# Optimization experiments

Hardware: AMD Instinct MI355X
Metric: run time of the kernel (lower is better)

The kernel has to match this reference:

```python
import jax, jax.numpy as jnp
import numpy as np

NUM_HEADS = 8
HEAD_DIM = 32  # in_channels // num_heads = 256 // 8


def setup_inputs() -> dict:
    key = jax.random.key(0)
    k1, k2, k3, k4 = jax.random.split(key, 4)
    B, C, H, W = 16, 256, 64, 64
    N = (H // 2) * (W // 2)  # 1024
    return {
        "x": jax.random.normal(k1, (B, C, H, W), dtype=jnp.float32),
        "w_qkv": jax.random.normal(k2, (3 * C, C), dtype=jnp.float32) * (1.0 / np.sqrt(C)),
        "b_qkv": jax.random.normal(k3, (3 * C,), dtype=jnp.float32) * 0.02,
        "pos_encoding": jax.random.normal(k4, (1, N, HEAD_DIM), dtype=jnp.float32) * 0.02,
    }


def reference(x, w_qkv, b_qkv, pos_encoding):
    B, C, H, W = x.shape
    Hp, Wp = H // 2, W // 2
    N = Hp * Wp
    # 1x1 conv: [B,C,H,W] -> [B,3C,H,W]
    y = jnp.einsum('bchw,oc->bohw', x, w_qkv) + b_qkv[None, :, None, None]
    # 2x2 max pool, stride 2
    y = y.reshape(B, 3 * C, Hp, 2, Wp, 2).max(axis=(3, 5))  # [B,3C,Hp,Wp]
    # split into q,k,v heads: channel order is (3, heads, head_dim)
    qkv = y.reshape(B, 3, NUM_HEADS, HEAD_DIM, N)
    qkv = qkv.transpose(1, 0, 2, 4, 3)  # [3,B,h,N,d]
    q, k, v = qkv[0], qkv[1], qkv[2]
    q = q + pos_encoding[:, None, :, :]  # broadcast over heads -> [B,h,N,d]
    scale = HEAD_DIM ** (-0.5)
    attn = jnp.einsum('bhnd,bhmd->bhnm', q, k) * scale
    attn = jax.nn.softmax(attn, axis=-1)
    out = jnp.einsum('bhnm,bhmd->bhnd', attn, v)  # [B,h,N,d]
    # transpose(2,3) then reshape -> [B, C, Hp, Wp]
    out = out.transpose(0, 1, 3, 2).reshape(B, C, Hp, Wp)
    return out
```

## Files before the change

### kernel.cpp

```cpp
#include <hip/hip_runtime.h>
#include <hip/hip_bf16.h>

typedef __bf16 bf16;
typedef bf16 bf16x8 __attribute__((ext_vector_type(8)));
typedef float f32x4 __attribute__((ext_vector_type(4)));
typedef float f32x16 __attribute__((ext_vector_type(16)));
typedef unsigned int u32;
typedef u32 u32x2 __attribute__((ext_vector_type(2)));
typedef u32 u32x4 __attribute__((ext_vector_type(4)));
typedef int i32x2 __attribute__((ext_vector_type(2)));


__device__ __forceinline__ u32 packbf2(float lo, float hi) {
    unsigned short a = __builtin_bit_cast(unsigned short, (bf16)lo);
    unsigned short b = __builtin_bit_cast(unsigned short, (bf16)hi);
    return (u32)a | ((u32)b << 16);
}

#if __has_builtin(__builtin_amdgcn_exp2f)
#define EXP2(x) __builtin_amdgcn_exp2f(x)
#else
#define EXP2(x) __expf((x)*0.69314718055994531f)
#endif

__device__ __forceinline__ i32x2 pl32swap(u32 a, u32 b) {
#if __has_builtin(__builtin_amdgcn_permlane32_swap)
    return __builtin_amdgcn_permlane32_swap((int)a, (int)b, false, false);
#else
    int lid = __builtin_amdgcn_mbcnt_hi(~0u, __builtin_amdgcn_mbcnt_lo(~0u, 0));
    u32 ax = (u32)__shfl_xor((int)a, 32);
    u32 bx = (u32)__shfl_xor((int)b, 32);
    i32x2 r;
    r.x = (int)(lid < 32 ? a : bx);
    r.y = (int)(lid < 32 ? ax : b);
    return r;
#endif
}

__device__ __forceinline__ f32x16 zero16() {
    f32x16 z;
#pragma unroll
    for (int i = 0; i < 16; ++i) z[i] = 0.f;
    return z;
}

__device__ __forceinline__ void gload_lds16(const bf16* gsrc, bf16* ldst) {
    __builtin_amdgcn_global_load_lds(
        (const __attribute__((address_space(1))) void*)gsrc,
        (__attribute__((address_space(3))) void*)ldst, 16, 0, 0);
}

#define MEMFENCE()                               \
    do {                                         \
        asm volatile("" ::: "memory");           \
        __builtin_amdgcn_sched_barrier(0);       \
    } while (0)

#define WAITV(N)                                                   \
    do {                                                           \
        asm volatile("s_waitcnt vmcnt(" #N ")" ::: "memory");      \
        __builtin_amdgcn_sched_barrier(0);                         \
    } while (0)

__global__ __launch_bounds__(256) void k_transpose_x(const float* __restrict__ x,
                                                     bf16* __restrict__ xt) {
    __shared__ __align__(16) bf16 tile[64][72];
    int b = blockIdx.z, cb = blockIdx.y, pb = blockIdx.x;
    int c0 = cb * 64, p0 = pb * 64;
    int t = threadIdx.x;
    int pr = (t & 15) * 4;
    int cr = t >> 4;
    const float* xp = x + ((size_t)(b * 256 + c0)) * 4096 + p0;
    for (int pass = 0; pass < 4; ++pass) {
        int c = cr + pass * 16;
        float4 v = *reinterpret_cast<const float4*>(xp + (size_t)c * 4096 + pr);
        tile[pr + 0][c] = (bf16)v.x;
        tile[pr + 1][c] = (bf16)v.y;
        tile[pr + 2][c] = (bf16)v.z;
        tile[pr + 3][c] = (bf16)v.w;
    }
    __syncthreads();
    bf16* op = xt + ((size_t)(b * 4096 + p0)) * 256 + c0;
    int c8 = (t & 7) * 8;
    int prow = t >> 3;
    for (int pass = 0; pass < 2; ++pass) {
        int p = prow + pass * 32;
        *reinterpret_cast<bf16x8*>(op + (size_t)p * 256 + c8) =
            *reinterpret_cast<const bf16x8*>(&tile[p][c8]);
    }
}

__global__ __launch_bounds__(256) void k_convert_w(const float* __restrict__ w,
                                                   bf16* __restrict__ wb) {
    int i = (blockIdx.x * 256 + threadIdx.x) * 8;
    float4 a = *reinterpret_cast<const float4*>(w + i);
    float4 b4 = *reinterpret_cast<const float4*>(w + i + 4);
    bf16x8 o;
    o[0] = (bf16)a.x;  o[1] = (bf16)a.y;  o[2] = (bf16)a.z;  o[3] = (bf16)a.w;
    o[4] = (bf16)b4.x; o[5] = (bf16)b4.y; o[6] = (bf16)b4.z; o[7] = (bf16)b4.w;
    *reinterpret_cast<bf16x8*>(wb + i) = o;
}

__global__ __launch_bounds__(256) void k_gemm_pool(const bf16* __restrict__ xt,
                                                   const bf16* __restrict__ wb,
                                                   const float* __restrict__ bias,
                                                   const float* __restrict__ pos,
                                                   bf16* __restrict__ Qb,
                                                   bf16* __restrict__ Kb,
                                                   bf16* __restrict__ Vb) {
    __shared__ __align__(16) bf16 bt[128 * 256];
    int b = blockIdx.y, nt = blockIdx.x;
    int p0 = nt * 128;
    int t = threadIdx.x;
    int w = t >> 6, lane = t & 63, g = lane >> 4, q = lane & 15;

    const bf16* xtp = xt + ((size_t)(b * 4096 + p0)) * 256;
    const bf16* wb_w = wb + (size_t)(w * 32) * 256;

    {
        int srow = t >> 5;
        int scb = t & 31;
        int wbase_row = w * 2;
#pragma unroll
        for (int pass = 0; pass < 16; ++pass) {
            int row = srow + pass * 8;
            int p = 2 * (row & 15) + ((row >> 4) & 1) + ((row >> 5) & 1) * 64 +
                    ((row >> 6) & 1) * 32;
            const bf16* gs = xtp + (size_t)p * 256 + ((scb ^ (row & 7)) << 3);
            gload_lds16(gs, bt + (pass * 8 + wbase_row) * 256);
        }
    }
    MEMFENCE();

    bf16x8 Ac[4], An[4];
#define LOADA(MT, KC, DST)                                                     \
    {                                                                          \
        _Pragma("unroll")                                                      \
        for (int ks = 0; ks < 2; ++ks)                                         \
            _Pragma("unroll")                                                  \
            for (int fr = 0; fr < 2; ++fr)                                     \
                DST[ks * 2 + fr] = *reinterpret_cast<const bf16x8*>(           \
                    wb_w + (size_t)((MT) * 128 + fr * 16 + q) * 256 +          \
                    (KC) * 64 + ks * 32 + g * 8);                              \
    }
    LOADA(0, 0, Ac);
    MEMFENCE();

    WAITV(4);
    __builtin_amdgcn_s_barrier();
    __builtin_amdgcn_sched_barrier(0);

    const float QSCALE = 0.2550406682649681f;

    for (int mt = 0; mt < 6; ++mt) {
        f32x4 acc[2][8];
#pragma unroll
        for (int fr = 0; fr < 2; ++fr)
#pragma unroll
            for (int fc = 0; fc < 8; ++fc) acc[fr][fc] = (f32x4){0.f, 0.f, 0.f, 0.f};

#pragma unroll
        for (int kc = 0; kc < 4; ++kc) {
            if (kc < 3) {
                LOADA(mt, kc + 1, An);
            } else if (mt < 5) {
                LOADA(mt + 1, 0, An);
            }
#pragma unroll
            for (int ks = 0; ks < 2; ++ks) {
#pragma unroll
                for (int fc = 0; fc < 8; ++fc) {
                    int co = kc * 64 + (((ks * 4 + g) ^ (q & 7)) << 3);
                    bf16x8 bfv = *reinterpret_cast<const bf16x8*>(
                        &bt[(fc * 16 + q) * 256 + co]);
                    acc[0][fc] = __builtin_amdgcn_mfma_f32_16x16x32_bf16(
                        Ac[ks * 2 + 0], bfv, acc[0][fc], 0, 0, 0);
                    acc[1][fc] = __builtin_amdgcn_mfma_f32_16x16x32_bf16(
                        Ac[ks * 2 + 1], bfv, acc[1][fc], 0, 0, 0);
                }
            }
#pragma unroll
            for (int i = 0; i < 4; ++i) Ac[i] = An[i];
        }

        int m0 = mt * 128;
        int sec = mt >> 1;
        int hh = ((m0 >> 5) + w) & 7;
        size_t bh = (size_t)(b * 8 + hh) * 32768;
#pragma unroll
        for (int fr = 0; fr < 2; ++fr) {
            int dbase = fr * 16 + g * 4;
            float4 bs = *reinterpret_cast<const float4*>(&bias[m0 + w * 32 + dbase]);
#pragma unroll
            for (int G = 0; G < 2; ++G) {
                int n_g = nt * 32 + G * 16 + q;
                float vm[4];
#pragma unroll
                for (int r = 0; r < 4; ++r) {
                    float a0 = fmaxf(acc[fr][4 * G + 0][r], acc[fr][4 * G + 1][r]);
                    float a1 = fmaxf(acc[fr][4 * G + 2][r], acc[fr][4 * G + 3][r]);
                    vm[r] = fmaxf(a0, a1) + ((const float*)&bs)[r];
                }
                if (sec == 0) {
                    float4 pv = *reinterpret_cast<const float4*>(
                        &pos[(size_t)n_g * 32 + dbase]);
                    u32x2 o2 = {packbf2((vm[0] + pv.x) * QSCALE, (vm[1] + pv.y) * QSCALE),
                                packbf2((vm[2] + pv.z) * QSCALE, (vm[3] + pv.w) * QSCALE)};
                    *reinterpret_cast<u32x2*>(Qb + bh + (size_t)n_g * 32 + dbase) = o2;
                } else if (sec == 1) {
                    u32x2 o2 = {packbf2(vm[0], vm[1]), packbf2(vm[2], vm[3])};
                    *reinterpret_cast<u32x2*>(Kb + bh + (size_t)n_g * 32 + dbase) = o2;
                } else {
#pragma unroll
                    for (int r = 0; r < 4; ++r)
                        Vb[bh + (size_t)(dbase + r) * 1024 + n_g] = (bf16)vm[r];
                }
            }
        }
    }
#undef LOADA
}

__global__ __launch_bounds__(256) void k_attn(const bf16* __restrict__ Q,
                                              const bf16* __restrict__ K,
                                              const bf16* __restrict__ V,
                                              float* __restrict__ out) {
    int h = blockIdx.x, b = blockIdx.y, qb = blockIdx.z;
    int t = threadIdx.x, w = t >> 6, lane = t & 63;
    int lq = lane & 31, hi = lane >> 5, hi8 = hi * 8;
    size_t bh = (size_t)b * 8 + h;
    const bf16* Qp = Q + bh * 32768;
    const bf16* Kp = K + bh * 32768;
    const bf16* Vp = V + bh * 32768;
    float* Op = out + ((size_t)(b * 256 + h * 32)) * 1024;
    int q0 = qb * 128 + w * 32;

    bf16x8 qf0 = *reinterpret_cast<const bf16x8*>(Qp + (size_t)(q0 + lq) * 32 + hi8);
    bf16x8 qf1 = *reinterpret_cast<const bf16x8*>(Qp + (size_t)(q0 + lq) * 32 + 16 + hi8);

    const bf16* kaddr = Kp + (size_t)lq * 32 + hi8;
    const bf16* vaddr = Vp + (size_t)lq * 1024 + hi8;

    f32x16 o = zero16();
    float run_s = 0.f;

    bf16x8 k0c = *reinterpret_cast<const bf16x8*>(kaddr);
    bf16x8 k1c = *reinterpret_cast<const bf16x8*>(kaddr + 16);
    bf16x8 v0c = *reinterpret_cast<const bf16x8*>(vaddr);
    bf16x8 v1c = *reinterpret_cast<const bf16x8*>(vaddr + 16);

    for (int kk = 0; kk < 32; ++kk) {
        int key0n = ((kk + 1) & 31) * 32;
        bf16x8 k0n = *reinterpret_cast<const bf16x8*>(kaddr + (size_t)key0n * 32);
        bf16x8 k1n = *reinterpret_cast<const bf16x8*>(kaddr + (size_t)key0n * 32 + 16);
        bf16x8 v0n = *reinterpret_cast<const bf16x8*>(vaddr + key0n);
        bf16x8 v1n = *reinterpret_cast<const bf16x8*>(vaddr + key0n + 16);

        f32x16 s = __builtin_amdgcn_mfma_f32_32x32x16_bf16(k0c, qf0, zero16(), 0, 0, 0);
        s = __builtin_amdgcn_mfma_f32_32x32x16_bf16(k1c, qf1, s, 0, 0, 0);

        float p[16];
#pragma unroll
        for (int r = 0; r < 16; ++r) p[r] = EXP2(s[r]);
        float ts = (((p[0] + p[1]) + (p[2] + p[3])) + ((p[4] + p[5]) + (p[6] + p[7]))) +
                   (((p[8] + p[9]) + (p[10] + p[11])) + ((p[12] + p[13]) + (p[14] + p[15])));
        run_s += ts;

        u32 pk0 = packbf2(p[0], p[1]),   pk1 = packbf2(p[2], p[3]);
        u32 pk2 = packbf2(p[4], p[5]),   pk3 = packbf2(p[6], p[7]);
        u32 pk4 = packbf2(p[8], p[9]),   pk5 = packbf2(p[10], p[11]);
        u32 pk6 = packbf2(p[12], p[13]), pk7 = packbf2(p[14], p[15]);

        i32x2 r02 = pl32swap(pk0, pk2);
        i32x2 r13 = pl32swap(pk1, pk3);
        i32x2 r46 = pl32swap(pk4, pk6);
        i32x2 r57 = pl32swap(pk5, pk7);

        u32x4 b0v = {(u32)r02.x, (u32)r13.x, (u32)r02.y, (u32)r13.y};
        u32x4 b1v = {(u32)r46.x, (u32)r57.x, (u32)r46.y, (u32)r57.y};
        bf16x8 pb0 = __builtin_bit_cast(bf16x8, b0v);
        bf16x8 pb1 = __builtin_bit_cast(bf16x8, b1v);

        o = __builtin_amdgcn_mfma_f32_32x32x16_bf16(v0c, pb0, o, 0, 0, 0);
        o = __builtin_amdgcn_mfma_f32_32x32x16_bf16(v1c, pb1, o, 0, 0, 0);

        k0c = k0n; k1c = k1n; v0c = v0n; v1c = v1n;
    }

    i32x2 rs = pl32swap(__builtin_bit_cast(u32, run_s), __builtin_bit_cast(u32, run_s));
    float tot = __builtin_bit_cast(float, (u32)rs.x) + __builtin_bit_cast(float, (u32)rs.y);
    float inv = 1.0f / tot;

#pragma unroll
    for (int r = 0; r < 16; ++r) {
        int dd = (r & 3) + 8 * (r >> 2) + 4 * hi;
        Op[(size_t)dd * 1024 + q0 + lq] = o[r] * inv;
    }
}

extern "C" void kernel_launch(void* const* d_in, const int* in_sizes, int n_in,
                              void* d_out, int out_size, void* d_ws, size_t ws_size,
                              hipStream_t stream) {
    const float* x = (const float*)d_in[0];
    const float* w = (const float*)d_in[1];
    const float* bias = (const float*)d_in[2];
    const float* pos = (const float*)d_in[3];
    float* outp = (float*)d_out;

    char* ws = (char*)d_ws;
    bf16* xt = (bf16*)(ws);
    bf16* wb = (bf16*)(ws + 33554432);
    bf16* Qb = (bf16*)(ws + 33947648);
    bf16* Kb = (bf16*)(ws + 42336256);
    bf16* Vb = (bf16*)(ws + 50724864);

    k_transpose_x<<<dim3(64, 4, 16), 256, 0, stream>>>(x, xt);
    k_convert_w<<<dim3(96), 256, 0, stream>>>(w, wb);
    k_gemm_pool<<<dim3(32, 16), 256, 0, stream>>>(xt, wb, bias, pos, Qb, Kb, Vb);
    k_attn<<<dim3(8, 16, 8), 256, 0, stream>>>(Qb, Kb, Vb, outp);
}
```

Measured before the change: 109.6 us.

## Split attention key range across wave pairs and combine partials in LDS

Each 32-query tile is now handled by two waves, each covering half of the keys. The block grows to 512 threads, and the partial outputs and row sums are merged through shared memory before normalisation. The goal is to shorten the serial 32-step key loop and raise the number of waves in flight, hiding load and MFMA latency. In exchange it adds an LDS round-trip, a block-wide barrier, and half the waves idle during the epilogue.

```diff
diff --git a/kernel.cpp b/kernel.cpp
--- a/kernel.cpp
+++ b/kernel.cpp
@@ -221,19 +221,21 @@
 #undef LOADA
 }
 
-__global__ __launch_bounds__(256) void k_attn(const bf16* __restrict__ Q,
-                                              const bf16* __restrict__ K,
-                                              const bf16* __restrict__ V,
-                                              float* __restrict__ out) {
+__global__ __launch_bounds__(512, 8) void k_attn(const bf16* __restrict__ Q,
+                                                 const bf16* __restrict__ K,
+                                                 const bf16* __restrict__ V,
+                                                 float* __restrict__ out) {
+    __shared__ float cmb[4][64][17];
     int h = blockIdx.x, b = blockIdx.y, qb = blockIdx.z;
     int t = threadIdx.x, w = t >> 6, lane = t & 63;
+    int pair = w >> 1, kh = w & 1;
     int lq = lane & 31, hi = lane >> 5, hi8 = hi * 8;
     size_t bh = (size_t)b * 8 + h;
     const bf16* Qp = Q + bh * 32768;
     const bf16* Kp = K + bh * 32768;
     const bf16* Vp = V + bh * 32768;
     float* Op = out + ((size_t)(b * 256 + h * 32)) * 1024;
-    int q0 = qb * 128 + w * 32;
+    int q0 = qb * 128 + pair * 32;
 
     bf16x8 qf0 = *reinterpret_cast<const bf16x8*>(Qp + (size_t)(q0 + lq) * 32 + hi8);
     bf16x8 qf1 = *reinterpret_cast<const bf16x8*>(Qp + (size_t)(q0 + lq) * 32 + 16 + hi8);
@@ -244,13 +246,15 @@
     f32x16 o = zero16();
     float run_s = 0.f;
 
-    bf16x8 k0c = *reinterpret_cast<const bf16x8*>(kaddr);
-    bf16x8 k1c = *reinterpret_cast<const bf16x8*>(kaddr + 16);
-    bf16x8 v0c = *reinterpret_cast<const bf16x8*>(vaddr);
-    bf16x8 v1c = *reinterpret_cast<const bf16x8*>(vaddr + 16);
-
-    for (int kk = 0; kk < 32; ++kk) {
-        int key0n = ((kk + 1) & 31) * 32;
+    int kbase = kh * 16;
+    int key00 = kbase * 32;
+    bf16x8 k0c = *reinterpret_cast<const bf16x8*>(kaddr + (size_t)key00 * 32);
+    bf16x8 k1c = *reinterpret_cast<const bf16x8*>(kaddr + (size_t)key00 * 32 + 16);
+    bf16x8 v0c = *reinterpret_cast<const bf16x8*>(vaddr + key00);
+    bf16x8 v1c = *reinterpret_cast<const bf16x8*>(vaddr + key00 + 16);
+
+    for (int i = 0; i < 16; ++i) {
+        int key0n = (kbase + ((i + 1) & 15)) * 32;
         bf16x8 k0n = *reinterpret_cast<const bf16x8*>(kaddr + (size_t)key0n * 32);
         bf16x8 k1n = *reinterpret_cast<const bf16x8*>(kaddr + (size_t)key0n * 32 + 16);
         bf16x8 v0n = *reinterpret_cast<const bf16x8*>(vaddr + key0n);
@@ -287,14 +291,26 @@
         k0c = k0n; k1c = k1n; v0c = v0n; v1c = v1n;
     }
 
-    i32x2 rs = pl32swap(__builtin_bit_cast(u32, run_s), __builtin_bit_cast(u32, run_s));
-    float tot = __builtin_bit_cast(float, (u32)rs.x) + __builtin_bit_cast(float, (u32)rs.y);
-    float inv = 1.0f / tot;
-
-#pragma unroll
-    for (int r = 0; r < 16; ++r) {
-        int dd = (r & 3) + 8 * (r >> 2) + 4 * hi;
-        Op[(size_t)dd * 1024 + q0 + lq] = o[r] * inv;
+    if (kh) {
+#pragma unroll
+        for (int r = 0; r < 16; ++r) cmb[pair][lane][r] = o[r];
+        cmb[pair][lane][16] = run_s;
+    }
+    __syncthreads();
+    if (!kh) {
+#pragma unroll
+        for (int r = 0; r < 16; ++r) o[r] += cmb[pair][lane][r];
+        run_s += cmb[pair][lane][16];
+
+        i32x2 rs = pl32swap(__builtin_bit_cast(u32, run_s), __builtin_bit_cast(u32, run_s));
+        float tot = __builtin_bit_cast(float, (u32)rs.x) + __builtin_bit_cast(float, (u32)rs.y);
+        float inv = 1.0f / tot;
+
+#pragma unroll
+        for (int r = 0; r < 16; ++r) {
+            int dd = (r & 3) + 8 * (r >> 2) + 4 * hi;
+            Op[(size_t)dd * 1024 + q0 + lq] = o[r] * inv;
+        }
     }
 }
 
@@ -317,5 +333,5 @@
     k_transpose_x<<<dim3(64, 4, 16), 256, 0, stream>>>(x, xt);
     k_convert_w<<<dim3(96), 256, 0, stream>>>(w, wb);
     k_gemm_pool<<<dim3(32, 16), 256, 0, stream>>>(xt, wb, bias, pos, Qb, Kb, Vb);
-    k_attn<<<dim3(8, 16, 8), 256, 0, stream>>>(Qb, Kb, Vb, outp);
-}
+    k_attn<<<dim3(8, 16, 8), 512, 0, stream>>>(Qb, Kb, Vb, outp);
+}
```

Result: no change. 110.9 us (+1.2%).

## Stage K/V tiles in double-buffered LDS via async global-to-LDS loads

Applied to the files above, without the earlier changes.

Each of the four waves used to load its own K and V fragments straight from global memory, so every wave fetched the same data redundantly. Now each wave async-loads one quarter of the 32-key K/V tile into a double-buffered LDS area with global_load_lds, and all waves read their fragments from LDS. This cuts global and L2 traffic by sharing the tile across waves. In exchange it adds two workgroup barriers and explicit vmcnt/lgkmcnt waits per iteration, which may serialize the MFMA work behind the loads.

```diff
diff --git a/kernel.cpp b/kernel.cpp
--- a/kernel.cpp
+++ b/kernel.cpp
@@ -59,6 +59,12 @@
 #define WAITV(N)                                                   \
     do {                                                           \
         asm volatile("s_waitcnt vmcnt(" #N ")" ::: "memory");      \
+        __builtin_amdgcn_sched_barrier(0);                         \
+    } while (0)
+
+#define WAITLGKM()                                                 \
+    do {                                                           \
+        asm volatile("s_waitcnt lgkmcnt(0)" ::: "memory");         \
         __builtin_amdgcn_sched_barrier(0);                         \
     } while (0)
 
@@ -225,6 +231,8 @@
                                               const bf16* __restrict__ K,
                                               const bf16* __restrict__ V,
                                               float* __restrict__ out) {
+    __shared__ __align__(16) bf16 kt[2][1024];
+    __shared__ __align__(16) bf16 vt[2][1024];
     int h = blockIdx.x, b = blockIdx.y, qb = blockIdx.z;
     int t = threadIdx.x, w = t >> 6, lane = t & 63;
     int lq = lane & 31, hi = lane >> 5, hi8 = hi * 8;
@@ -238,23 +246,42 @@
     bf16x8 qf0 = *reinterpret_cast<const bf16x8*>(Qp + (size_t)(q0 + lq) * 32 + hi8);
     bf16x8 qf1 = *reinterpret_cast<const bf16x8*>(Qp + (size_t)(q0 + lq) * 32 + 16 + hi8);
 
-    const bf16* kaddr = Kp + (size_t)lq * 32 + hi8;
-    const bf16* vaddr = Vp + (size_t)lq * 1024 + hi8;
+    int sc = ((w & 1) << 1) + (lane >> 5);
+    int srow = lane & 31;
+    const bf16* sgK = Kp + (size_t)srow * 32 + sc * 8;
+    const bf16* sgV = Vp + (size_t)srow * 1024 + sc * 8;
+    int sdst = (w & 1) * 512;
+
+#define STAGEKV(BB, KK)                                                        \
+    do {                                                                       \
+        int key0_ = (KK) * 32;                                                 \
+        if (w < 2) gload_lds16(sgK + (size_t)key0_ * 32, &kt[BB][sdst]);       \
+        else       gload_lds16(sgV + key0_, &vt[BB][sdst]);                    \
+    } while (0)
+
+    STAGEKV(0, 0);
+    MEMFENCE();
+    STAGEKV(1, 1);
+    MEMFENCE();
 
     f32x16 o = zero16();
     float run_s = 0.f;
 
-    bf16x8 k0c = *reinterpret_cast<const bf16x8*>(kaddr);
-    bf16x8 k1c = *reinterpret_cast<const bf16x8*>(kaddr + 16);
-    bf16x8 v0c = *reinterpret_cast<const bf16x8*>(vaddr);
-    bf16x8 v1c = *reinterpret_cast<const bf16x8*>(vaddr + 16);
-
     for (int kk = 0; kk < 32; ++kk) {
-        int key0n = ((kk + 1) & 31) * 32;
-        bf16x8 k0n = *reinterpret_cast<const bf16x8*>(kaddr + (size_t)key0n * 32);
-        bf16x8 k1n = *reinterpret_cast<const bf16x8*>(kaddr + (size_t)key0n * 32 + 16);
-        bf16x8 v0n = *reinterpret_cast<const bf16x8*>(vaddr + key0n);
-        bf16x8 v1n = *reinterpret_cast<const bf16x8*>(vaddr + key0n + 16);
+        int cur = kk & 1;
+        if (kk < 31) { WAITV(1); } else { WAITV(0); }
+        __builtin_amdgcn_s_barrier();
+        __builtin_amdgcn_sched_barrier(0);
+
+        bf16x8 k0c = *reinterpret_cast<const bf16x8*>(&kt[cur][hi * 256 + lq * 8]);
+        bf16x8 k1c = *reinterpret_cast<const bf16x8*>(&kt[cur][(2 + hi) * 256 + lq * 8]);
+        bf16x8 v0c = *reinterpret_cast<const bf16x8*>(&vt[cur][hi * 256 + lq * 8]);
+        bf16x8 v1c = *reinterpret_cast<const bf16x8*>(&vt[cur][(2 + hi) * 256 + lq * 8]);
+        WAITLGKM();
+        __builtin_amdgcn_s_barrier();
+        __builtin_amdgcn_sched_barrier(0);
+        if (kk < 30) STAGEKV(cur, kk + 2);
+        MEMFENCE();
 
         f32x16 s = __builtin_amdgcn_mfma_f32_32x32x16_bf16(k0c, qf0, zero16(), 0, 0, 0);
         s = __builtin_amdgcn_mfma_f32_32x32x16_bf16(k1c, qf1, s, 0, 0, 0);
@@ -283,9 +310,8 @@
 
         o = __builtin_amdgcn_mfma_f32_32x32x16_bf16(v0c, pb0, o, 0, 0, 0);
         o = __builtin_amdgcn_mfma_f32_32x32x16_bf16(v1c, pb1, o, 0, 0, 0);
-
-        k0c = k0n; k1c = k1n; v0c = v0n; v1c = v1n;
-    }
+    }
+#undef STAGEKV
 
     i32x2 rs = pl32swap(__builtin_bit_cast(u32, run_s), __builtin_bit_cast(u32, run_s));
     float tot = __builtin_bit_cast(float, (u32)rs.x) + __builtin_bit_cast(float, (u32)rs.y);
```

Result: faster. 103.3 us (-5.7%).
